# Optimization experiments

Measured on AMD Instinct MI355X. Metric: run time of the kernel, lower is better.

## Reference

```python
import jax, jax.numpy as jnp
import numpy as np

N_NODES = 100000
N_EDGES = 3200000
N_GRAPHS = 512


def setup_inputs() -> dict:
    key = jax.random.key(0)
    ks = jax.random.split(key, 8)
    x = jax.random.normal(ks[0], (N_NODES, 3), dtype=jnp.float32)
    W1 = jax.random.normal(ks[1], (3, 32), dtype=jnp.float32) * (1.0 / np.sqrt(3))
    b1 = jnp.zeros((32,), dtype=jnp.float32)
    W2 = jax.random.normal(ks[2], (32, 64), dtype=jnp.float32) * (1.0 / np.sqrt(32))
    b2 = jnp.zeros((64,), dtype=jnp.float32)
    W3 = jax.random.normal(ks[3], (64, 64), dtype=jnp.float32) * (1.0 / np.sqrt(64))
    b3 = jnp.zeros((64,), dtype=jnp.float32)
    Wc = jax.random.normal(ks[4], (128, 2), dtype=jnp.float32) * (1.0 / np.sqrt(128))
    bc = jnp.zeros((2,), dtype=jnp.float32)
    edge_index = jax.random.randint(ks[5], (2, N_EDGES), 0, N_NODES, dtype=jnp.int64)
    # sorted, evenly-split graph assignment -> every graph non-empty (needed for max pool)
    batch = (jnp.arange(N_NODES, dtype=jnp.int64) * N_GRAPHS) // N_NODES
    return {"x": x, "W1": W1, "b1": b1, "W2": W2, "b2": b2, "W3": W3, "b3": b3,
            "Wc": Wc, "bc": bc, "edge_index": edge_index, "batch": batch}


def _gcn_norm(edge_index, n_nodes):
    # add self loops, then symmetric normalization: deg^-1/2[src]*deg^-1/2[dst]
    loops = jnp.arange(n_nodes, dtype=edge_index.dtype)
    src = jnp.concatenate([edge_index[0], loops])
    dst = jnp.concatenate([edge_index[1], loops])
    deg = jax.ops.segment_sum(jnp.ones_like(dst, dtype=jnp.float32), dst,
                              num_segments=n_nodes)
    dinv = jax.lax.rsqrt(deg)  # deg >= 1 thanks to self loops
    norm = dinv[src] * dinv[dst]
    return src, dst, norm


def _gcn_conv(x, W, b, src, dst, norm, n_nodes):
    h = x @ W                                   # [N, out]
    msg = h[src] * norm[:, None]                # gather + edge scale  [E, out]
    agg = jax.ops.segment_sum(msg, dst, num_segments=n_nodes)  # scatter-add
    return agg + b


def reference(x, W1, b1, W2, b2, W3, b3, Wc, bc, edge_index, batch):
    n = x.shape[0]
    src, dst, norm = _gcn_norm(edge_index, n)
    h = jax.nn.relu(_gcn_conv(x, W1, b1, src, dst, norm, n))
    h = jax.nn.relu(_gcn_conv(h, W2, b2, src, dst, norm, n))
    h = _gcn_conv(h, W3, b3, src, dst, norm, n)
    # global max / mean pool over graphs
    x_max = jax.ops.segment_max(h, batch, num_segments=N_GRAPHS)
    sums = jax.ops.segment_sum(h, batch, num_segments=N_GRAPHS)
    cnts = jax.ops.segment_sum(jnp.ones((n, 1), dtype=h.dtype), batch,
                               num_segments=N_GRAPHS)
    x_mean = sums / jnp.maximum(cnts, 1.0)
    x_comb = jnp.concatenate([x_max, x_mean], axis=1)   # [G, 128]
    logits = x_comb @ Wc + bc                           # [G, 2]
    return jax.nn.softmax(logits, axis=1)
```

## Files before the change

### kernel.cpp

```cpp
#include <hip/hip_runtime.h>
#include <math.h>

#define TPB 256
#define TPB_H 512
#define TPB_BIN 1024
#define CSR_TPB 1024
#define NB_MAX 512
#define BKT_SHIFT 8
#define BKT_NODES 256
#define BIN_CHUNK 8192

__device__ inline float bfLO(unsigned u) { return __uint_as_float(u << 16); }
__device__ inline float bfHI(unsigned u) { return __uint_as_float(u & 0xffff0000u); }
__device__ inline unsigned short f2bf(float f) {
    unsigned int x = __float_as_uint(f);
    return (unsigned short)((x + 0x7fffu + ((x >> 16) & 1u)) >> 16);
}

__global__ void k_hist_coarse(const int* __restrict__ dst, int* __restrict__ bucketCnt,
                              int e, int nb) {
    __shared__ int h[NB_MAX];
    for (int i = threadIdx.x; i < nb; i += TPB_H) h[i] = 0;
    __syncthreads();
    int e4 = e >> 2;
    const int4* d4 = (const int4*)dst;
    for (long long i = (long long)blockIdx.x * TPB_H + threadIdx.x; i < e4;
         i += (long long)gridDim.x * TPB_H) {
        int4 v = d4[i];
        atomicAdd(&h[v.x >> BKT_SHIFT], 1);
        atomicAdd(&h[v.y >> BKT_SHIFT], 1);
        atomicAdd(&h[v.z >> BKT_SHIFT], 1);
        atomicAdd(&h[v.w >> BKT_SHIFT], 1);
    }
    if (blockIdx.x == 0)
        for (int i = (e4 << 2) + threadIdx.x; i < e; i += TPB_H)
            atomicAdd(&h[dst[i] >> BKT_SHIFT], 1);
    __syncthreads();
    for (int i = threadIdx.x; i < nb; i += TPB_H)
        if (h[i]) atomicAdd(&bucketCnt[i], h[i]);
}

__global__ void k_scanb(const int* __restrict__ cnt, int* __restrict__ boff,
                        int* __restrict__ bcur, int* __restrict__ off_nodes,
                        int nb, int e, int n) {
    __shared__ int lds[NB_MAX];
    int t = threadIdx.x;
    int v = (t < nb) ? cnt[t] : 0;
    lds[t] = v;
    __syncthreads();
    for (int d = 1; d < NB_MAX; d <<= 1) {
// ... 57 lines not shown
        if (t < BKT_NODES && t >= d) x = offl[t - d];
        __syncthreads();
        if (t < BKT_NODES) offl[t] += x;
        __syncthreads();
    }
    if (t < BKT_NODES) {
        int excl = offl[t] - v;
        cur[t] = excl;
        int nd = nbase + t;
        if (nd < n) {
            off_nodes[nd] = e0 + excl;
            dinv[nd] = rsqrtf((float)(v + 1));
        }
    }
    __syncthreads();
    for (int e = e0 + t; e < e1; e += CSR_TPB) {
        unsigned p = pairs[e];
        int l = (int)(p >> 24);
        int pos = e0 + atomicAdd(&cur[l], 1);
        csr[pos] = (int)(p & 0xffffffu);
    }
}

__global__ void k_scale3(const float* __restrict__ x, const float* __restrict__ dinv,
                         float* __restrict__ xp, int n3) {
    int t = blockIdx.x * TPB + threadIdx.x;
    if (t >= n3) return;
    xp[t] = x[t] * dinv[t / 3];
}

__global__ void k_g3mm1(const int* __restrict__ off, const int* __restrict__ csr,
                        const float* __restrict__ dinv, const float* __restrict__ xp,
                        const float* __restrict__ W1, const float* __restrict__ b1,
                        unsigned short* __restrict__ T1, int n) {
    __shared__ float w1s[96];
    __shared__ float b1s[32];
    if (threadIdx.x < 96) w1s[threadIdx.x] = W1[threadIdx.x];
    if (threadIdx.x < 32) b1s[threadIdx.x] = b1[threadIdx.x];
    __syncthreads();
    int i = blockIdx.x * TPB + threadIdx.x;
    if (i >= n) return;
    float s0 = xp[i * 3], s1 = xp[i * 3 + 1], s2 = xp[i * 3 + 2];
    int e = off[i], e1 = off[i + 1];
    for (; e + 3 < e1; e += 4) {
        int sa = csr[e], sb = csr[e + 1], sc = csr[e + 2], sd = csr[e + 3];
        float a0 = xp[sa * 3], a1 = xp[sa * 3 + 1], a2 = xp[sa * 3 + 2];
        float c0 = xp[sb * 3], c1 = xp[sb * 3 + 1], c2 = xp[sb * 3 + 2];
        float d0 = xp[sc * 3], d1 = xp[sc * 3 + 1], d2 = xp[sc * 3 + 2];
        float f0 = xp[sd * 3], f1 = xp[sd * 3 + 1], f2 = xp[sd * 3 + 2];
        s0 += a0 + c0 + d0 + f0;
        s1 += a1 + c1 + d1 + f1;
        s2 += a2 + c2 + d2 + f2;
    }
    for (; e < e1; ++e) {
        int s = csr[e];
        s0 += xp[s * 3]; s1 += xp[s * 3 + 1]; s2 += xp[s * 3 + 2];
    }
    float di = dinv[i];
    s0 *= di; s1 *= di; s2 *= di;
    unsigned outw[16];
#pragma unroll
    for (int fp = 0; fp < 16; fp++) {
        float h0 = fmaf(s0, w1s[2 * fp], fmaf(s1, w1s[32 + 2 * fp], fmaf(s2, w1s[64 + 2 * fp], b1s[2 * fp])));
        float h1 = fmaf(s0, w1s[2 * fp + 1], fmaf(s1, w1s[32 + 2 * fp + 1], fmaf(s2, w1s[64 + 2 * fp + 1], b1s[2 * fp + 1])));
        h0 = fmaxf(h0, 0.0f) * di;
        h1 = fmaxf(h1, 0.0f) * di;
        outw[fp] = (unsigned)f2bf(h0) | ((unsigned)f2bf(h1) << 16);
    }
    uint4* o = (uint4*)(T1 + (size_t)i * 32);
    o[0] = make_uint4(outw[0], outw[1], outw[2], outw[3]);
    o[1] = make_uint4(outw[4], outw[5], outw[6], outw[7]);
    o[2] = make_uint4(outw[8], outw[9], outw[10], outw[11]);
    o[3] = make_uint4(outw[12], outw[13], outw[14], outw[15]);
}

#define ACC8(v) do { \
    a0 += bfLO((v).x); a1 += bfHI((v).x); a2 += bfLO((v).y); a3 += bfHI((v).y); \
    a4 += bfLO((v).z); a5 += bfHI((v).z); a6 += bfLO((v).w); a7 += bfHI((v).w); } while (0)

__global__ void k_gather32b(const int* __restrict__ off, const int* __restrict__ csr,
                            const float* __restrict__ dinv, const unsigned short* __restrict__ T,
                            float* __restrict__ G, int n) {
    int w = (blockIdx.x * TPB + threadIdx.x) >> 6;
    if (w >= n) return;
    int lane = threadIdx.x & 63;
    int grp = lane >> 2, q = lane & 3;
    float a0 = 0, a1 = 0, a2 = 0, a3 = 0, a4 = 0, a5 = 0, a6 = 0, a7 = 0;
    if (grp == 0) {
        uint4 v = *(const uint4*)(T + ((size_t)w << 5) + (q << 3));
        ACC8(v);
    }
    int e = off[w] + grp, e1 = off[w + 1];
    for (; e + 16 < e1; e += 32) {
        int s0 = csr[e], s1 = csr[e + 16];
        uint4 v0 = *(const uint4*)(T + ((size_t)s0 << 5) + (q << 3));
        uint4 v1 = *(const uint4*)(T + ((size_t)s1 << 5) + (q << 3));
        ACC8(v0); ACC8(v1);
    }
    if (e < e1) {
        int s = csr[e];
        uint4 v = *(const uint4*)(T + ((size_t)s << 5) + (q << 3));
        ACC8(v);
    }
#pragma unroll
    for (int m = 4; m < 64; m <<= 1) {
        a0 += __shfl_xor(a0, m); a1 += __shfl_xor(a1, m);
        a2 += __shfl_xor(a2, m); a3 += __shfl_xor(a3, m);
        a4 += __shfl_xor(a4, m); a5 += __shfl_xor(a5, m);
        a6 += __shfl_xor(a6, m); a7 += __shfl_xor(a7, m);
    }
    if (grp == 0) {
        float di = dinv[w];
        float* g = G + ((size_t)w << 5) + (q << 3);
        *(float4*)g = make_float4(a0 * di, a1 * di, a2 * di, a3 * di);
        *(float4*)(g + 4) = make_float4(a4 * di, a5 * di, a6 * di, a7 * di);
    }
}

__global__ void k_mm2(const float* __restrict__ G, const float* __restrict__ W,
                      const float* __restrict__ b, const float* __restrict__ dinv,
                      unsigned short* __restrict__ T, int n) {
    int i = blockIdx.x * TPB + threadIdx.x;
    if (i >= n) return;
    float gr[32];
    const float4* g4 = (const float4*)(G + (size_t)i * 32);
#pragma unroll
    for (int c = 0; c < 8; c++) {
        float4 v = g4[c];
        gr[4 * c] = v.x; gr[4 * c + 1] = v.y; gr[4 * c + 2] = v.z; gr[4 * c + 3] = v.w;
    }
    float di = dinv[i];
    uint2* o = (uint2*)(T + (size_t)i * 64);
    for (int fc = 0; fc < 16; fc++) {
        const float* bb = b + 4 * fc;
        float a0 = bb[0], a1 = bb[1], a2 = bb[2], a3 = bb[3];
#pragma unroll
        for (int k = 0; k < 32; k++) {
            const float* wr = W + k * 64 + 4 * fc;
            float g = gr[k];
            a0 = fmaf(g, wr[0], a0);
            a1 = fmaf(g, wr[1], a1);
            a2 = fmaf(g, wr[2], a2);
            a3 = fmaf(g, wr[3], a3);
        }
        a0 = fmaxf(a0, 0.0f) * di; a1 = fmaxf(a1, 0.0f) * di;
        a2 = fmaxf(a2, 0.0f) * di; a3 = fmaxf(a3, 0.0f) * di;
        o[fc] = make_uint2((unsigned)f2bf(a0) | ((unsigned)f2bf(a1) << 16),
                           (unsigned)f2bf(a2) | ((unsigned)f2bf(a3) << 16));
    }
}

__global__ void k_gather64b(const int* __restrict__ off, const int* __restrict__ csr,
                            const float* __restrict__ dinv, const unsigned short* __restrict__ T,
                            float* __restrict__ G, int n) {
    int w = (blockIdx.x * TPB + threadIdx.x) >> 6;
    if (w >= n) return;
    int lane = threadIdx.x & 63;
    int grp = lane >> 3, q = lane & 7;
    float a0 = 0, a1 = 0, a2 = 0, a3 = 0, a4 = 0, a5 = 0, a6 = 0, a7 = 0;
    if (grp == 0) {
        uint4 v = *(const uint4*)(T + ((size_t)w << 6) + (q << 3));
        ACC8(v);
    }
    int e = off[w] + grp, e1 = off[w + 1];
    for (; e + 24 < e1; e += 32) {
        int s0 = csr[e], s1 = csr[e + 8], s2 = csr[e + 16], s3 = csr[e + 24];
        uint4 v0 = *(const uint4*)(T + ((size_t)s0 << 6) + (q << 3));
        uint4 v1 = *(const uint4*)(T + ((size_t)s1 << 6) + (q << 3));
        uint4 v2 = *(const uint4*)(T + ((size_t)s2 << 6) + (q << 3));
        uint4 v3 = *(const uint4*)(T + ((size_t)s3 << 6) + (q << 3));
        ACC8(v0); ACC8(v1); ACC8(v2); ACC8(v3);
    }
    for (; e < e1; e += 8) {
        int s = csr[e];
        uint4 v = *(const uint4*)(T + ((size_t)s << 6) + (q << 3));
        ACC8(v);
    }
#pragma unroll
    for (int m = 8; m < 64; m <<= 1) {
        a0 += __shfl_xor(a0, m); a1 += __shfl_xor(a1, m);
        a2 += __shfl_xor(a2, m); a3 += __shfl_xor(a3, m);
        a4 += __shfl_xor(a4, m); a5 += __shfl_xor(a5, m);
        a6 += __shfl_xor(a6, m); a7 += __shfl_xor(a7, m);
    }
    if (grp == 0) {
        float di = dinv[w];
        float* g = G + ((size_t)w << 6) + (q << 3);
        *(float4*)g = make_float4(a0 * di, a1 * di, a2 * di, a3 * di);
        *(float4*)(g + 4) = make_float4(a4 * di, a5 * di, a6 * di, a7 * di);
    }
}

__global__ void k_mm3(const float* __restrict__ G, const float* __restrict__ W,
                      const float* __restrict__ b, float* __restrict__ H, int n) {
    int i = blockIdx.x * TPB + threadIdx.x;
    if (i >= n) return;
    float gr[64];
    const float4* g4 = (const float4*)(G + (size_t)i * 64);
#pragma unroll
    for (int c = 0; c < 16; c++) {
        float4 v = g4[c];
        gr[4 * c] = v.x; gr[4 * c + 1] = v.y; gr[4 * c + 2] = v.z; gr[4 * c + 3] = v.w;
    }
    float4* h4 = (float4*)(H + (size_t)i * 64);
    for (int fc = 0; fc < 16; fc++) {
        const float* bb = b + 4 * fc;
        float a0 = bb[0], a1 = bb[1], a2 = bb[2], a3 = bb[3];
#pragma unroll
        for (int k = 0; k < 64; k++) {
            const float* wr = W + k * 64 + 4 * fc;
            float g = gr[k];
            a0 = fmaf(g, wr[0], a0);
            a1 = fmaf(g, wr[1], a1);
            a2 = fmaf(g, wr[2], a2);
            a3 = fmaf(g, wr[3], a3);
        }
        h4[fc] = make_float4(a0, a1, a2, a3);
    }
}

__global__ void k_pool(const float* __restrict__ H, const float* __restrict__ Wc,
                       const float* __restrict__ bc, float* __restrict__ out,
                       int n, int g_total) {
    int g = blockIdx.x;
    int f = threadIdx.x & 63;
    int c = threadIdx.x >> 6;
    long long start = ((long long)g * n + g_total - 1) / g_total;
    long long end = ((long long)(g + 1) * n + g_total - 1) / g_total;
    float mx = -INFINITY, sm = 0.0f;
    for (long long i = start + c; i < end; i += 4) {
        float v = H[(i << 6) | f];
        mx = fmaxf(mx, v);
        sm += v;
    }
    __shared__ float smax[4][64], ssum[4][64], slog[2];
    smax[c][f] = mx; ssum[c][f] = sm;
    __syncthreads();
    if (c == 0) {
        mx = fmaxf(fmaxf(smax[0][f], smax[1][f]), fmaxf(smax[2][f], smax[3][f]));
        sm = ssum[0][f] + ssum[1][f] + ssum[2][f] + ssum[3][f];
        long long cnt = end - start;
        smax[0][f] = mx;
        ssum[0][f] = sm / (float)(cnt > 0 ? cnt : 1);
    }
    __syncthreads();
    if (threadIdx.x < 2) {
        int cls = threadIdx.x;
        float l = bc[cls];
        for (int k = 0; k < 64; k++)
            l += smax[0][k] * Wc[k * 2 + cls] + ssum[0][k] * Wc[(64 + k) * 2 + cls];
        slog[cls] = l;
    }
    __syncthreads();
    if (threadIdx.x == 0) {
        float m = fmaxf(slog[0], slog[1]);
        float e0 = expf(slog[0] - m), e1 = expf(slog[1] - m);
        float inv = 1.0f / (e0 + e1);
        out[g * 2 + 0] = e0 * inv;
        out[g * 2 + 1] = e1 * inv;
    }
}

extern "C" void kernel_launch(void* const* d_in, const int* in_sizes, int n_in,
                              void* d_out, int out_size, void* d_ws, size_t ws_size,
                              hipStream_t stream) {
    const float* x  = (const float*)d_in[0];
    const float* W1 = (const float*)d_in[1];
    const float* b1 = (const float*)d_in[2];
    const float* W2 = (const float*)d_in[3];
    const float* b2 = (const float*)d_in[4];
    const float* W3 = (const float*)d_in[5];
    const float* b3 = (const float*)d_in[6];
    const float* Wc = (const float*)d_in[7];
    const float* bc = (const float*)d_in[8];
    const int*   ei = (const int*)d_in[9];

    const int N = in_sizes[0] / 3;
    const int E = in_sizes[9] / 2;
    const int G = out_size / 2;
    const int* src = ei;
    const int* dst = ei + E;

    char* ws = (char*)d_ws;
    size_t off_b = 0;
    auto alloc = [&](size_t bytes) {
        size_t o = off_b;
        off_b = (off_b + bytes + 255) & ~(size_t)255;
        return (void*)(ws + o);
    };
    float* dinv      = (float*)alloc((size_t)N * 4);
    int*   off       = (int*)alloc((size_t)(N + 1) * 4);
    int*   bucketCnt = (int*)alloc((NB_MAX + 1) * 4);
    int*   bucketOff = (int*)alloc((NB_MAX + 1) * 4);
    int*   bucketCur = (int*)alloc((NB_MAX + 1) * 4);
    int*   csr       = (int*)alloc((size_t)E * 4);
    float* xp        = (float*)alloc((size_t)N * 3 * 4);
    size_t bufA_sz   = (size_t)N * 64 * 4;
    if ((size_t)E * 4 > bufA_sz) bufA_sz = (size_t)E * 4;
    float* bufA      = (float*)alloc(bufA_sz);
    float* bufB      = (float*)alloc((size_t)N * 64 * 4);

    unsigned* pairs = (unsigned*)bufA;
    float* G1 = bufA;
    float* G2 = bufA;
    unsigned short* T1 = (unsigned short*)bufB;
    unsigned short* T2 = (unsigned short*)bufB;
    float* H  = bufB;

    auto cdiv = [](long long a, long long b) { return (int)((a + b - 1) / b); };
    const int nb = cdiv(N, BKT_NODES);

    hipMemsetAsync(bucketCnt, 0, (size_t)nb * 4, stream);
    k_hist_coarse<<<1024, TPB_H, 0, stream>>>(dst, bucketCnt, E, nb);
    k_scanb<<<1, NB_MAX, 0, stream>>>(bucketCnt, bucketOff, bucketCur, off, nb, E, N);
    k_bin_pairs<<<cdiv(E, BIN_CHUNK), TPB_BIN, 0, stream>>>(src, dst, bucketCur, pairs, E, nb);
    k_bucket_csr<<<nb, CSR_TPB, 0, stream>>>(pairs, bucketOff, off, dinv, csr, N);

    k_scale3<<<cdiv((long long)N * 3, TPB), TPB, 0, stream>>>(x, dinv, xp, N * 3);
    k_g3mm1<<<cdiv(N, TPB), TPB, 0, stream>>>(off, csr, dinv, xp, W1, b1, T1, N);

    k_gather32b<<<cdiv((long long)N * 64, TPB), TPB, 0, stream>>>(off, csr, dinv, T1, G1, N);
    k_mm2<<<cdiv(N, TPB), TPB, 0, stream>>>(G1, W2, b2, dinv, T2, N);

    k_gather64b<<<cdiv((long long)N * 64, TPB), TPB, 0, stream>>>(off, csr, dinv, T2, G2, N);
    k_mm3<<<cdiv(N, TPB), TPB, 0, stream>>>(G2, W3, b3, H, N);

    k_pool<<<G, TPB, 0, stream>>>(H, Wc, bc, (float*)d_out, N, G);
}
```

Measured before the change: 307.6 us.

## Quantize gathered GCN features to per-row int8 with float scales

Intermediate node features fed to the two neighbour-gather kernels are now stored as unsigned 8-bit values with a per-node float scale instead of bf16, halving the bytes fetched per edge. The gather kernels are reorganised so each lane reads 16 bytes covering 16 features, with fewer lanes per row and more edges in flight per wavefront. Each gathered row now also needs an extra scale load and integer-to-float conversions. Accuracy drops to 7-bit per-row quantization, which may or may not stay within tolerance.

```diff
diff --git a/kernel.cpp b/kernel.cpp
--- a/kernel.cpp
+++ b/kernel.cpp
@@ -9,13 +9,6 @@
 #define BKT_SHIFT 8
 #define BKT_NODES 256
 #define BIN_CHUNK 8192
-
-__device__ inline float bfLO(unsigned u) { return __uint_as_float(u << 16); }
-__device__ inline float bfHI(unsigned u) { return __uint_as_float(u & 0xffff0000u); }
-__device__ inline unsigned short f2bf(float f) {
-    unsigned int x = __float_as_uint(f);
-    return (unsigned short)((x + 0x7fffu + ((x >> 16) & 1u)) >> 16);
-}
 
 __global__ void k_hist_coarse(const int* __restrict__ dst, int* __restrict__ bucketCnt,
                               int e, int nb) {
@@ -139,7 +132,7 @@
 __global__ void k_g3mm1(const int* __restrict__ off, const int* __restrict__ csr,
                         const float* __restrict__ dinv, const float* __restrict__ xp,
                         const float* __restrict__ W1, const float* __restrict__ b1,
-                        unsigned short* __restrict__ T1, int n) {
+                        unsigned char* __restrict__ T1, float* __restrict__ sc1, int n) {
     __shared__ float w1s[96];
     __shared__ float b1s[32];
     if (threadIdx.x < 96) w1s[threadIdx.x] = W1[threadIdx.x];
@@ -165,68 +158,80 @@
     }
     float di = dinv[i];
     s0 *= di; s1 *= di; s2 *= di;
-    unsigned outw[16];
-#pragma unroll
-    for (int fp = 0; fp < 16; fp++) {
-        float h0 = fmaf(s0, w1s[2 * fp], fmaf(s1, w1s[32 + 2 * fp], fmaf(s2, w1s[64 + 2 * fp], b1s[2 * fp])));
-        float h1 = fmaf(s0, w1s[2 * fp + 1], fmaf(s1, w1s[32 + 2 * fp + 1], fmaf(s2, w1s[64 + 2 * fp + 1], b1s[2 * fp + 1])));
-        h0 = fmaxf(h0, 0.0f) * di;
-        h1 = fmaxf(h1, 0.0f) * di;
-        outw[fp] = (unsigned)f2bf(h0) | ((unsigned)f2bf(h1) << 16);
+    float vals[32];
+    float mx = 0.0f;
+#pragma unroll
+    for (int f = 0; f < 32; f++) {
+        float h = fmaf(s0, w1s[f], fmaf(s1, w1s[32 + f], fmaf(s2, w1s[64 + f], b1s[f])));
+        h = fmaxf(h, 0.0f) * di;
+        vals[f] = h;
+        mx = fmaxf(mx, h);
+    }
+    float inv = 127.0f / fmaxf(mx, 1e-20f);
+    sc1[i] = mx * (1.0f / 127.0f);
+    unsigned pw[8];
+#pragma unroll
+    for (int u = 0; u < 8; u++) {
+        unsigned q0 = (unsigned)__float2int_rn(vals[4 * u] * inv);
+        unsigned q1 = (unsigned)__float2int_rn(vals[4 * u + 1] * inv);
+        unsigned q2 = (unsigned)__float2int_rn(vals[4 * u + 2] * inv);
+        unsigned q3 = (unsigned)__float2int_rn(vals[4 * u + 3] * inv);
+        pw[u] = q0 | (q1 << 8) | (q2 << 16) | (q3 << 24);
     }
     uint4* o = (uint4*)(T1 + (size_t)i * 32);
-    o[0] = make_uint4(outw[0], outw[1], outw[2], outw[3]);
-    o[1] = make_uint4(outw[4], outw[5], outw[6], outw[7]);
-    o[2] = make_uint4(outw[8], outw[9], outw[10], outw[11]);
-    o[3] = make_uint4(outw[12], outw[13], outw[14], outw[15]);
-}
-
-#define ACC8(v) do { \
-    a0 += bfLO((v).x); a1 += bfHI((v).x); a2 += bfLO((v).y); a3 += bfHI((v).y); \
-    a4 += bfLO((v).z); a5 += bfHI((v).z); a6 += bfLO((v).w); a7 += bfHI((v).w); } while (0)
-
-__global__ void k_gather32b(const int* __restrict__ off, const int* __restrict__ csr,
-                            const float* __restrict__ dinv, const unsigned short* __restrict__ T,
-                            float* __restrict__ G, int n) {
+    o[0] = make_uint4(pw[0], pw[1], pw[2], pw[3]);
+    o[1] = make_uint4(pw[4], pw[5], pw[6], pw[7]);
+}
+
+#define QACC4(word, base) do { \
+    a[(base) + 0] = fmaf(s, (float)((word) & 0xffu), a[(base) + 0]); \
+    a[(base) + 1] = fmaf(s, (float)(((word) >> 8) & 0xffu), a[(base) + 1]); \
+    a[(base) + 2] = fmaf(s, (float)(((word) >> 16) & 0xffu), a[(base) + 2]); \
+    a[(base) + 3] = fmaf(s, (float)((word) >> 24), a[(base) + 3]); \
+} while (0)
+
+#define QACC16(v) do { QACC4((v).x, 0); QACC4((v).y, 4); QACC4((v).z, 8); QACC4((v).w, 12); } while (0)
+
+__global__ void k_gather32i(const int* __restrict__ off, const int* __restrict__ csr,
+                            const float* __restrict__ dinv, const unsigned char* __restrict__ T,
+                            const float* __restrict__ sc, float* __restrict__ G, int n) {
     int w = (blockIdx.x * TPB + threadIdx.x) >> 6;
     if (w >= n) return;
     int lane = threadIdx.x & 63;
-    int grp = lane >> 2, q = lane & 3;
-    float a0 = 0, a1 = 0, a2 = 0, a3 = 0, a4 = 0, a5 = 0, a6 = 0, a7 = 0;
+    int grp = lane >> 1, q = lane & 1;
+    float a[16];
+#pragma unroll
+    for (int j = 0; j < 16; j++) a[j] = 0.0f;
     if (grp == 0) {
-        uint4 v = *(const uint4*)(T + ((size_t)w << 5) + (q << 3));
-        ACC8(v);
+        float s = sc[w];
+        uint4 v = *(const uint4*)(T + ((size_t)w << 5) + (q << 4));
+        QACC16(v);
     }
     int e = off[w] + grp, e1 = off[w + 1];
-    for (; e + 16 < e1; e += 32) {
-        int s0 = csr[e], s1 = csr[e + 16];
-        uint4 v0 = *(const uint4*)(T + ((size_t)s0 << 5) + (q << 3));
-        uint4 v1 = *(const uint4*)(T + ((size_t)s1 << 5) + (q << 3));
-        ACC8(v0); ACC8(v1);
-    }
-    if (e < e1) {
-        int s = csr[e];
-        uint4 v = *(const uint4*)(T + ((size_t)s << 5) + (q << 3));
-        ACC8(v);
-    }
-#pragma unroll
-    for (int m = 4; m < 64; m <<= 1) {
-        a0 += __shfl_xor(a0, m); a1 += __shfl_xor(a1, m);
-        a2 += __shfl_xor(a2, m); a3 += __shfl_xor(a3, m);
-        a4 += __shfl_xor(a4, m); a5 += __shfl_xor(a5, m);
-        a6 += __shfl_xor(a6, m); a7 += __shfl_xor(a7, m);
+    for (; e < e1; e += 32) {
+        int si = csr[e];
+        float s = sc[si];
+        uint4 v = *(const uint4*)(T + ((size_t)si << 5) + (q << 4));
+        QACC16(v);
+    }
+#pragma unroll
+    for (int m = 2; m < 64; m <<= 1) {
+#pragma unroll
+        for (int j = 0; j < 16; j++) a[j] += __shfl_xor(a[j], m);
     }
     if (grp == 0) {
         float di = dinv[w];
-        float* g = G + ((size_t)w << 5) + (q << 3);
-        *(float4*)g = make_float4(a0 * di, a1 * di, a2 * di, a3 * di);
-        *(float4*)(g + 4) = make_float4(a4 * di, a5 * di, a6 * di, a7 * di);
+        float4* g = (float4*)(G + ((size_t)w << 5) + (q << 4));
+#pragma unroll
+        for (int c = 0; c < 4; c++)
+            g[c] = make_float4(a[4 * c] * di, a[4 * c + 1] * di,
+                               a[4 * c + 2] * di, a[4 * c + 3] * di);
     }
 }
 
 __global__ void k_mm2(const float* __restrict__ G, const float* __restrict__ W,
                       const float* __restrict__ b, const float* __restrict__ dinv,
-                      unsigned short* __restrict__ T, int n) {
+                      unsigned char* __restrict__ T, float* __restrict__ sc2, int n) {
     int i = blockIdx.x * TPB + threadIdx.x;
     if (i >= n) return;
     float gr[32];
@@ -237,7 +242,9 @@
         gr[4 * c] = v.x; gr[4 * c + 1] = v.y; gr[4 * c + 2] = v.z; gr[4 * c + 3] = v.w;
     }
     float di = dinv[i];
-    uint2* o = (uint2*)(T + (size_t)i * 64);
+    float vals[64];
+    float mx = 0.0f;
+#pragma unroll
     for (int fc = 0; fc < 16; fc++) {
         const float* bb = b + 4 * fc;
         float a0 = bb[0], a1 = bb[1], a2 = bb[2], a3 = bb[3];
@@ -252,49 +259,70 @@
         }
         a0 = fmaxf(a0, 0.0f) * di; a1 = fmaxf(a1, 0.0f) * di;
         a2 = fmaxf(a2, 0.0f) * di; a3 = fmaxf(a3, 0.0f) * di;
-        o[fc] = make_uint2((unsigned)f2bf(a0) | ((unsigned)f2bf(a1) << 16),
-                           (unsigned)f2bf(a2) | ((unsigned)f2bf(a3) << 16));
-    }
-}
-
-__global__ void k_gather64b(const int* __restrict__ off, const int* __restrict__ csr,
-                            const float* __restrict__ dinv, const unsigned short* __restrict__ T,
-                            float* __restrict__ G, int n) {
+        vals[4 * fc] = a0; vals[4 * fc + 1] = a1;
+        vals[4 * fc + 2] = a2; vals[4 * fc + 3] = a3;
+        mx = fmaxf(mx, fmaxf(fmaxf(a0, a1), fmaxf(a2, a3)));
+    }
+    float inv = 127.0f / fmaxf(mx, 1e-20f);
+    sc2[i] = mx * (1.0f / 127.0f);
+    unsigned pw[16];
+#pragma unroll
+    for (int u = 0; u < 16; u++) {
+        unsigned q0 = (unsigned)__float2int_rn(vals[4 * u] * inv);
+        unsigned q1 = (unsigned)__float2int_rn(vals[4 * u + 1] * inv);
+        unsigned q2 = (unsigned)__float2int_rn(vals[4 * u + 2] * inv);
+        unsigned q3 = (unsigned)__float2int_rn(vals[4 * u + 3] * inv);
+        pw[u] = q0 | (q1 << 8) | (q2 << 16) | (q3 << 24);
+    }
+    uint4* o = (uint4*)(T + (size_t)i * 64);
+    o[0] = make_uint4(pw[0], pw[1], pw[2], pw[3]);
+    o[1] = make_uint4(pw[4], pw[5], pw[6], pw[7]);
+    o[2] = make_uint4(pw[8], pw[9], pw[10], pw[11]);
+    o[3] = make_uint4(pw[12], pw[13], pw[14], pw[15]);
+}
+
+__global__ void k_gather64i(const int* __restrict__ off, const int* __restrict__ csr,
+                            const float* __restrict__ dinv, const unsigned char* __restrict__ T,
+                            const float* __restrict__ sc, float* __restrict__ G, int n) {
     int w = (blockIdx.x * TPB + threadIdx.x) >> 6;
     if (w >= n) return;
     int lane = threadIdx.x & 63;
-    int grp = lane >> 3, q = lane & 7;
-    float a0 = 0, a1 = 0, a2 = 0, a3 = 0, a4 = 0, a5 = 0, a6 = 0, a7 = 0;
+    int grp = lane >> 2, q = lane & 3;
+    float a[16];
+#pragma unroll
+    for (int j = 0; j < 16; j++) a[j] = 0.0f;
     if (grp == 0) {
-        uint4 v = *(const uint4*)(T + ((size_t)w << 6) + (q << 3));
-        ACC8(v);
+        float s = sc[w];
+        uint4 v = *(const uint4*)(T + ((size_t)w << 6) + (q << 4));
+        QACC16(v);
     }
     int e = off[w] + grp, e1 = off[w + 1];
-    for (; e + 24 < e1; e += 32) {
-        int s0 = csr[e], s1 = csr[e + 8], s2 = csr[e + 16], s3 = csr[e + 24];
-        uint4 v0 = *(const uint4*)(T + ((size_t)s0 << 6) + (q << 3));
-        uint4 v1 = *(const uint4*)(T + ((size_t)s1 << 6) + (q << 3));
-        uint4 v2 = *(const uint4*)(T + ((size_t)s2 << 6) + (q << 3));
-        uint4 v3 = *(const uint4*)(T + ((size_t)s3 << 6) + (q << 3));
-        ACC8(v0); ACC8(v1); ACC8(v2); ACC8(v3);
-    }
-    for (; e < e1; e += 8) {
-        int s = csr[e];
-        uint4 v = *(const uint4*)(T + ((size_t)s << 6) + (q << 3));
-        ACC8(v);
-    }
-#pragma unroll
-    for (int m = 8; m < 64; m <<= 1) {
-        a0 += __shfl_xor(a0, m); a1 += __shfl_xor(a1, m);
-        a2 += __shfl_xor(a2, m); a3 += __shfl_xor(a3, m);
-        a4 += __shfl_xor(a4, m); a5 += __shfl_xor(a5, m);
-        a6 += __shfl_xor(a6, m); a7 += __shfl_xor(a7, m);
+    for (; e + 16 < e1; e += 32) {
+        int s0i = csr[e], s1i = csr[e + 16];
+        float sA = sc[s0i], sB = sc[s1i];
+        uint4 v0 = *(const uint4*)(T + ((size_t)s0i << 6) + (q << 4));
+        uint4 v1 = *(const uint4*)(T + ((size_t)s1i << 6) + (q << 4));
+        { float s = sA; QACC16(v0); }
+        { float s = sB; QACC16(v1); }
+    }
+    if (e < e1) {
+        int si = csr[e];
+        float s = sc[si];
+        uint4 v = *(const uint4*)(T + ((size_t)si << 6) + (q << 4));
+        QACC16(v);
+    }
+#pragma unroll
+    for (int m = 4; m < 64; m <<= 1) {
+#pragma unroll
+        for (int j = 0; j < 16; j++) a[j] += __shfl_xor(a[j], m);
     }
     if (grp == 0) {
         float di = dinv[w];
-        float* g = G + ((size_t)w << 6) + (q << 3);
-        *(float4*)g = make_float4(a0 * di, a1 * di, a2 * di, a3 * di);
-        *(float4*)(g + 4) = make_float4(a4 * di, a5 * di, a6 * di, a7 * di);
+        float4* g = (float4*)(G + ((size_t)w << 6) + (q << 4));
+#pragma unroll
+        for (int c = 0; c < 4; c++)
+            g[c] = make_float4(a[4 * c] * di, a[4 * c + 1] * di,
+                               a[4 * c + 2] * di, a[4 * c + 3] * di);
     }
 }
 
@@ -402,6 +430,8 @@
     int*   bucketCur = (int*)alloc((NB_MAX + 1) * 4);
     int*   csr       = (int*)alloc((size_t)E * 4);
     float* xp        = (float*)alloc((size_t)N * 3 * 4);
+    float* sc1       = (float*)alloc((size_t)N * 4);
+    float* sc2       = (float*)alloc((size_t)N * 4);
     size_t bufA_sz   = (size_t)N * 64 * 4;
     if ((size_t)E * 4 > bufA_sz) bufA_sz = (size_t)E * 4;
     float* bufA      = (float*)alloc(bufA_sz);
@@ -410,9 +440,9 @@
     unsigned* pairs = (unsigned*)bufA;
     float* G1 = bufA;
     float* G2 = bufA;
-    unsigned short* T1 = (unsigned short*)bufB;
-    unsigned short* T2 = (unsigned short*)bufB;
-    float* H  = bufB;
+    unsigned char* T1 = (unsigned char*)bufB;
+    unsigned char* T2 = (unsigned char*)bufB;
+    float* H  = (float*)bufB;
 
     auto cdiv = [](long long a, long long b) { return (int)((a + b - 1) / b); };
     const int nb = cdiv(N, BKT_NODES);
@@ -424,12 +454,12 @@
     k_bucket_csr<<<nb, CSR_TPB, 0, stream>>>(pairs, bucketOff, off, dinv, csr, N);
 
     k_scale3<<<cdiv((long long)N * 3, TPB), TPB, 0, stream>>>(x, dinv, xp, N * 3);
-    k_g3mm1<<<cdiv(N, TPB), TPB, 0, stream>>>(off, csr, dinv, xp, W1, b1, T1, N);
-
-    k_gather32b<<<cdiv((long long)N * 64, TPB), TPB, 0, stream>>>(off, csr, dinv, T1, G1, N);
-    k_mm2<<<cdiv(N, TPB), TPB, 0, stream>>>(G1, W2, b2, dinv, T2, N);
-
-    k_gather64b<<<cdiv((long long)N * 64, TPB), TPB, 0, stream>>>(off, csr, dinv, T2, G2, N);
+    k_g3mm1<<<cdiv(N, TPB), TPB, 0, stream>>>(off, csr, dinv, xp, W1, b1, T1, sc1, N);
+
+    k_gather32i<<<cdiv((long long)N * 64, TPB), TPB, 0, stream>>>(off, csr, dinv, T1, sc1, G1, N);
+    k_mm2<<<cdiv(N, TPB), TPB, 0, stream>>>(G1, W2, b2, dinv, T2, sc2, N);
+
+    k_gather64i<<<cdiv((long long)N * 64, TPB), TPB, 0, stream>>>(off, csr, dinv, T2, sc2, G2, N);
     k_mm3<<<cdiv(N, TPB), TPB, 0, stream>>>(G2, W3, b3, H, N);
 
     k_pool<<<G, TPB, 0, stream>>>(H, Wc, bc, (float*)d_out, N, G);
```

After: 339.7 us. +10.4%, slower.

## Quantize layer-2 features to int8 with per-node scale and fuse pooling into mm3

Applied to the files above, without the earlier changes.

Layer-2 node features are now stored as int8 with a per-node scale instead of bf16, which halves the bytes each edge gather reads in the 64-wide aggregation. The third matmul is fused with global max/mean pooling through shared-memory and global atomics, so the N×64 hidden buffer is never written to memory or read back. A small classifier kernel then finishes the softmax. Int8 quantization adds error and float atomic sums make the result order-dependent.

```diff
diff --git a/kernel.cpp b/kernel.cpp
--- a/kernel.cpp
+++ b/kernel.cpp
@@ -15,6 +15,14 @@
 __device__ inline unsigned short f2bf(float f) {
     unsigned int x = __float_as_uint(f);
     return (unsigned short)((x + 0x7fffu + ((x >> 16) & 1u)) >> 16);
+}
+__device__ inline unsigned fkey(float f) {
+    int s = __float_as_int(f);
+    return (unsigned)(s >= 0 ? (s | 0x80000000) : ~s);
+}
+__device__ inline float funkey(unsigned k) {
+    int s = (k & 0x80000000u) ? (int)(k & 0x7fffffffu) : ~(int)k;
+    return __int_as_float(s);
 }
 
 __global__ void k_hist_coarse(const int* __restrict__ dst, int* __restrict__ bucketCnt,
@@ -226,7 +234,7 @@
 
 __global__ void k_mm2(const float* __restrict__ G, const float* __restrict__ W,
                       const float* __restrict__ b, const float* __restrict__ dinv,
-                      unsigned short* __restrict__ T, int n) {
+                      unsigned char* __restrict__ T, float* __restrict__ sc2, int n) {
     int i = blockIdx.x * TPB + threadIdx.x;
     if (i >= n) return;
     float gr[32];
@@ -237,7 +245,9 @@
         gr[4 * c] = v.x; gr[4 * c + 1] = v.y; gr[4 * c + 2] = v.z; gr[4 * c + 3] = v.w;
     }
     float di = dinv[i];
-    uint2* o = (uint2*)(T + (size_t)i * 64);
+    float vals[64];
+    float mx = 0.0f;
+#pragma unroll
     for (int fc = 0; fc < 16; fc++) {
         const float* bb = b + 4 * fc;
         float a0 = bb[0], a1 = bb[1], a2 = bb[2], a3 = bb[3];
@@ -252,114 +262,156 @@
         }
         a0 = fmaxf(a0, 0.0f) * di; a1 = fmaxf(a1, 0.0f) * di;
         a2 = fmaxf(a2, 0.0f) * di; a3 = fmaxf(a3, 0.0f) * di;
-        o[fc] = make_uint2((unsigned)f2bf(a0) | ((unsigned)f2bf(a1) << 16),
-                           (unsigned)f2bf(a2) | ((unsigned)f2bf(a3) << 16));
-    }
-}
-
-__global__ void k_gather64b(const int* __restrict__ off, const int* __restrict__ csr,
-                            const float* __restrict__ dinv, const unsigned short* __restrict__ T,
-                            float* __restrict__ G, int n) {
+        vals[4 * fc] = a0; vals[4 * fc + 1] = a1;
+        vals[4 * fc + 2] = a2; vals[4 * fc + 3] = a3;
+        mx = fmaxf(mx, fmaxf(fmaxf(a0, a1), fmaxf(a2, a3)));
+    }
+    float inv = 127.0f / fmaxf(mx, 1e-20f);
+    sc2[i] = mx * (1.0f / 127.0f);
+    unsigned pw[16];
+#pragma unroll
+    for (int u = 0; u < 16; u++) {
+        unsigned q0 = (unsigned)__float2int_rn(vals[4 * u] * inv);
+        unsigned q1 = (unsigned)__float2int_rn(vals[4 * u + 1] * inv);
+        unsigned q2 = (unsigned)__float2int_rn(vals[4 * u + 2] * inv);
+        unsigned q3 = (unsigned)__float2int_rn(vals[4 * u + 3] * inv);
+        pw[u] = q0 | (q1 << 8) | (q2 << 16) | (q3 << 24);
+    }
+    uint4* o = (uint4*)(T + (size_t)i * 64);
+    o[0] = make_uint4(pw[0], pw[1], pw[2], pw[3]);
+    o[1] = make_uint4(pw[4], pw[5], pw[6], pw[7]);
+    o[2] = make_uint4(pw[8], pw[9], pw[10], pw[11]);
+    o[3] = make_uint4(pw[12], pw[13], pw[14], pw[15]);
+}
+
+#define QACC4(word, base) do { \
+    a[(base) + 0] = fmaf(s, (float)((word) & 0xffu), a[(base) + 0]); \
+    a[(base) + 1] = fmaf(s, (float)(((word) >> 8) & 0xffu), a[(base) + 1]); \
+    a[(base) + 2] = fmaf(s, (float)(((word) >> 16) & 0xffu), a[(base) + 2]); \
+    a[(base) + 3] = fmaf(s, (float)((word) >> 24), a[(base) + 3]); \
+} while (0)
+
+#define QACC16(v) do { QACC4((v).x, 0); QACC4((v).y, 4); QACC4((v).z, 8); QACC4((v).w, 12); } while (0)
+
+__global__ void k_gather64i(const int* __restrict__ off, const int* __restrict__ csr,
+                            const float* __restrict__ dinv, const unsigned char* __restrict__ T,
+                            const float* __restrict__ sc, float* __restrict__ G, int n) {
     int w = (blockIdx.x * TPB + threadIdx.x) >> 6;
     if (w >= n) return;
     int lane = threadIdx.x & 63;
-    int grp = lane >> 3, q = lane & 7;
-    float a0 = 0, a1 = 0, a2 = 0, a3 = 0, a4 = 0, a5 = 0, a6 = 0, a7 = 0;
+    int grp = lane >> 2, q = lane & 3;
+    float a[16];
+#pragma unroll
+    for (int j = 0; j < 16; j++) a[j] = 0.0f;
     if (grp == 0) {
-        uint4 v = *(const uint4*)(T + ((size_t)w << 6) + (q << 3));
-        ACC8(v);
+        float s = sc[w];
+        uint4 v = *(const uint4*)(T + ((size_t)w << 6) + (q << 4));
+        QACC16(v);
     }
     int e = off[w] + grp, e1 = off[w + 1];
-    for (; e + 24 < e1; e += 32) {
-        int s0 = csr[e], s1 = csr[e + 8], s2 = csr[e + 16], s3 = csr[e + 24];
-        uint4 v0 = *(const uint4*)(T + ((size_t)s0 << 6) + (q << 3));
-        uint4 v1 = *(const uint4*)(T + ((size_t)s1 << 6) + (q << 3));
-        uint4 v2 = *(const uint4*)(T + ((size_t)s2 << 6) + (q << 3));
-        uint4 v3 = *(const uint4*)(T + ((size_t)s3 << 6) + (q << 3));
-        ACC8(v0); ACC8(v1); ACC8(v2); ACC8(v3);
-    }
-    for (; e < e1; e += 8) {
-        int s = csr[e];
-        uint4 v = *(const uint4*)(T + ((size_t)s << 6) + (q << 3));
-        ACC8(v);
-    }
-#pragma unroll
-    for (int m = 8; m < 64; m <<= 1) {
-        a0 += __shfl_xor(a0, m); a1 += __shfl_xor(a1, m);
-        a2 += __shfl_xor(a2, m); a3 += __shfl_xor(a3, m);
-        a4 += __shfl_xor(a4, m); a5 += __shfl_xor(a5, m);
-        a6 += __shfl_xor(a6, m); a7 += __shfl_xor(a7, m);
+    for (; e + 16 < e1; e += 32) {
+        int s0i = csr[e], s1i = csr[e + 16];
+        float sA = sc[s0i], sB = sc[s1i];
+        uint4 v0 = *(const uint4*)(T + ((size_t)s0i << 6) + (q << 4));
+        uint4 v1 = *(const uint4*)(T + ((size_t)s1i << 6) + (q << 4));
+        { float s = sA; QACC16(v0); }
+        { float s = sB; QACC16(v1); }
+    }
+    if (e < e1) {
+        int si = csr[e];
+        float s = sc[si];
+        uint4 v = *(const uint4*)(T + ((size_t)si << 6) + (q << 4));
+        QACC16(v);
+    }
+#pragma unroll
+    for (int m = 4; m < 64; m <<= 1) {
+#pragma unroll
+        for (int j = 0; j < 16; j++) a[j] += __shfl_xor(a[j], m);
     }
     if (grp == 0) {
         float di = dinv[w];
-        float* g = G + ((size_t)w << 6) + (q << 3);
-        *(float4*)g = make_float4(a0 * di, a1 * di, a2 * di, a3 * di);
-        *(float4*)(g + 4) = make_float4(a4 * di, a5 * di, a6 * di, a7 * di);
-    }
-}
-
-__global__ void k_mm3(const float* __restrict__ G, const float* __restrict__ W,
-                      const float* __restrict__ b, float* __restrict__ H, int n) {
-    int i = blockIdx.x * TPB + threadIdx.x;
-    if (i >= n) return;
-    float gr[64];
-    const float4* g4 = (const float4*)(G + (size_t)i * 64);
-#pragma unroll
-    for (int c = 0; c < 16; c++) {
-        float4 v = g4[c];
-        gr[4 * c] = v.x; gr[4 * c + 1] = v.y; gr[4 * c + 2] = v.z; gr[4 * c + 3] = v.w;
-    }
-    float4* h4 = (float4*)(H + (size_t)i * 64);
-    for (int fc = 0; fc < 16; fc++) {
-        const float* bb = b + 4 * fc;
-        float a0 = bb[0], a1 = bb[1], a2 = bb[2], a3 = bb[3];
-#pragma unroll
-        for (int k = 0; k < 64; k++) {
-            const float* wr = W + k * 64 + 4 * fc;
-            float g = gr[k];
-            a0 = fmaf(g, wr[0], a0);
-            a1 = fmaf(g, wr[1], a1);
-            a2 = fmaf(g, wr[2], a2);
-            a3 = fmaf(g, wr[3], a3);
+        float4* g = (float4*)(G + ((size_t)w << 6) + (q << 4));
+#pragma unroll
+        for (int c = 0; c < 4; c++)
+            g[c] = make_float4(a[4 * c] * di, a[4 * c + 1] * di,
+                               a[4 * c + 2] * di, a[4 * c + 3] * di);
+    }
+}
+
+__global__ void k_mm3pool(const float* __restrict__ G, const float* __restrict__ W,
+                          const float* __restrict__ b, unsigned* __restrict__ gmaxk,
+                          float* __restrict__ gsum, int n, int g_total) {
+    __shared__ unsigned lmk[4][64];
+    __shared__ float lsm[4][64];
+    int t = threadIdx.x;
+    int i0 = blockIdx.x * TPB;
+    int i = i0 + t;
+    int gfirst = (int)(((long long)i0 * g_total) / n);
+    lmk[t >> 6][t & 63] = 0u;
+    lsm[t >> 6][t & 63] = 0.0f;
+    __syncthreads();
+    if (i < n) {
+        float gr[64];
+        const float4* g4 = (const float4*)(G + (size_t)i * 64);
+#pragma unroll
+        for (int c = 0; c < 16; c++) {
+            float4 v = g4[c];
+            gr[4 * c] = v.x; gr[4 * c + 1] = v.y; gr[4 * c + 2] = v.z; gr[4 * c + 3] = v.w;
         }
-        h4[fc] = make_float4(a0, a1, a2, a3);
-    }
-}
-
-__global__ void k_pool(const float* __restrict__ H, const float* __restrict__ Wc,
-                       const float* __restrict__ bc, float* __restrict__ out,
-                       int n, int g_total) {
+        int gl = (int)(((long long)i * g_total) / n) - gfirst;
+        for (int fc = 0; fc < 16; fc++) {
+            const float* bb = b + 4 * fc;
+            float a0 = bb[0], a1 = bb[1], a2 = bb[2], a3 = bb[3];
+#pragma unroll
+            for (int k = 0; k < 64; k++) {
+                const float* wr = W + k * 64 + 4 * fc;
+                float g = gr[k];
+                a0 = fmaf(g, wr[0], a0);
+                a1 = fmaf(g, wr[1], a1);
+                a2 = fmaf(g, wr[2], a2);
+                a3 = fmaf(g, wr[3], a3);
+            }
+            atomicMax(&lmk[gl][4 * fc + 0], fkey(a0));
+            atomicMax(&lmk[gl][4 * fc + 1], fkey(a1));
+            atomicMax(&lmk[gl][4 * fc + 2], fkey(a2));
+            atomicMax(&lmk[gl][4 * fc + 3], fkey(a3));
+            atomicAdd(&lsm[gl][4 * fc + 0], a0);
+            atomicAdd(&lsm[gl][4 * fc + 1], a1);
+            atomicAdd(&lsm[gl][4 * fc + 2], a2);
+            atomicAdd(&lsm[gl][4 * fc + 3], a3);
+        }
+    }
+    __syncthreads();
+    int sgl = t >> 6, sf = t & 63;
+    unsigned mk = lmk[sgl][sf];
+    float sm = lsm[sgl][sf];
+    if (mk != 0u) {
+        int g = gfirst + sgl;
+        atomicMax(&gmaxk[g * 64 + sf], mk);
+        atomicAdd(&gsum[g * 64 + sf], sm);
+    }
+}
+
+__global__ void k_cls(const unsigned* __restrict__ gmaxk, const float* __restrict__ gsum,
+                      const float* __restrict__ Wc, const float* __restrict__ bc,
+                      float* __restrict__ out, int n, int g_total) {
     int g = blockIdx.x;
-    int f = threadIdx.x & 63;
-    int c = threadIdx.x >> 6;
+    int f = threadIdx.x;
     long long start = ((long long)g * n + g_total - 1) / g_total;
     long long end = ((long long)(g + 1) * n + g_total - 1) / g_total;
-    float mx = -INFINITY, sm = 0.0f;
-    for (long long i = start + c; i < end; i += 4) {
-        float v = H[(i << 6) | f];
-        mx = fmaxf(mx, v);
-        sm += v;
-    }
-    __shared__ float smax[4][64], ssum[4][64], slog[2];
-    smax[c][f] = mx; ssum[c][f] = sm;
-    __syncthreads();
-    if (c == 0) {
-        mx = fmaxf(fmaxf(smax[0][f], smax[1][f]), fmaxf(smax[2][f], smax[3][f]));
-        sm = ssum[0][f] + ssum[1][f] + ssum[2][f] + ssum[3][f];
-        long long cnt = end - start;
-        smax[0][f] = mx;
-        ssum[0][f] = sm / (float)(cnt > 0 ? cnt : 1);
-    }
-    __syncthreads();
-    if (threadIdx.x < 2) {
-        int cls = threadIdx.x;
-        float l = bc[cls];
+    float cnt = (float)(end - start);
+    __shared__ float smax[64], smean[64], slog[2];
+    smax[f] = funkey(gmaxk[g * 64 + f]);
+    smean[f] = gsum[g * 64 + f] / fmaxf(cnt, 1.0f);
+    __syncthreads();
+    if (f < 2) {
+        float l = bc[f];
         for (int k = 0; k < 64; k++)
-            l += smax[0][k] * Wc[k * 2 + cls] + ssum[0][k] * Wc[(64 + k) * 2 + cls];
-        slog[cls] = l;
-    }
-    __syncthreads();
-    if (threadIdx.x == 0) {
+            l += smax[k] * Wc[k * 2 + f] + smean[k] * Wc[(64 + k) * 2 + f];
+        slog[f] = l;
+    }
+    __syncthreads();
+    if (f == 0) {
         float m = fmaxf(slog[0], slog[1]);
         float e0 = expf(slog[0] - m), e1 = expf(slog[1] - m);
         float inv = 1.0f / (e0 + e1);
@@ -395,24 +447,26 @@
         off_b = (off_b + bytes + 255) & ~(size_t)255;
         return (void*)(ws + o);
     };
-    float* dinv      = (float*)alloc((size_t)N * 4);
-    int*   off       = (int*)alloc((size_t)(N + 1) * 4);
-    int*   bucketCnt = (int*)alloc((NB_MAX + 1) * 4);
-    int*   bucketOff = (int*)alloc((NB_MAX + 1) * 4);
-    int*   bucketCur = (int*)alloc((NB_MAX + 1) * 4);
-    int*   csr       = (int*)alloc((size_t)E * 4);
-    float* xp        = (float*)alloc((size_t)N * 3 * 4);
-    size_t bufA_sz   = (size_t)N * 64 * 4;
+    float*    dinv      = (float*)alloc((size_t)N * 4);
+    int*      off       = (int*)alloc((size_t)(N + 1) * 4);
+    int*      bucketCnt = (int*)alloc((NB_MAX + 1) * 4);
+    int*      bucketOff = (int*)alloc((NB_MAX + 1) * 4);
+    int*      bucketCur = (int*)alloc((NB_MAX + 1) * 4);
+    int*      csr       = (int*)alloc((size_t)E * 4);
+    float*    xp        = (float*)alloc((size_t)N * 3 * 4);
+    float*    sc2       = (float*)alloc((size_t)N * 4);
+    unsigned* gmaxk     = (unsigned*)alloc((size_t)G * 64 * 4);
+    float*    gsum      = (float*)alloc((size_t)G * 64 * 4);
+    size_t bufA_sz = (size_t)N * 64 * 4;
     if ((size_t)E * 4 > bufA_sz) bufA_sz = (size_t)E * 4;
-    float* bufA      = (float*)alloc(bufA_sz);
-    float* bufB      = (float*)alloc((size_t)N * 64 * 4);
+    float* bufA = (float*)alloc(bufA_sz);
+    float* bufB = (float*)alloc((size_t)N * 64);
 
     unsigned* pairs = (unsigned*)bufA;
     float* G1 = bufA;
     float* G2 = bufA;
     unsigned short* T1 = (unsigned short*)bufB;
-    unsigned short* T2 = (unsigned short*)bufB;
-    float* H  = bufB;
+    unsigned char*  T2 = (unsigned char*)bufB;
 
     auto cdiv = [](long long a, long long b) { return (int)((a + b - 1) / b); };
     const int nb = cdiv(N, BKT_NODES);
@@ -427,10 +481,12 @@
     k_g3mm1<<<cdiv(N, TPB), TPB, 0, stream>>>(off, csr, dinv, xp, W1, b1, T1, N);
 
     k_gather32b<<<cdiv((long long)N * 64, TPB), TPB, 0, stream>>>(off, csr, dinv, T1, G1, N);
-    k_mm2<<<cdiv(N, TPB), TPB, 0, stream>>>(G1, W2, b2, dinv, T2, N);
-
-    k_gather64b<<<cdiv((long long)N * 64, TPB), TPB, 0, stream>>>(off, csr, dinv, T2, G2, N);
-    k_mm3<<<cdiv(N, TPB), TPB, 0, stream>>>(G2, W3, b3, H, N);
-
-    k_pool<<<G, TPB, 0, stream>>>(H, Wc, bc, (float*)d_out, N, G);
-}
+    k_mm2<<<cdiv(N, TPB), TPB, 0, stream>>>(G1, W2, b2, dinv, T2, sc2, N);
+
+    k_gather64i<<<cdiv((long long)N * 64, TPB), TPB, 0, stream>>>(off, csr, dinv, T2, sc2, G2, N);
+    hipMemsetAsync(gmaxk, 0, (size_t)G * 64 * 4, stream);
+    hipMemsetAsync(gsum, 0, (size_t)G * 64 * 4, stream);
+    k_mm3pool<<<cdiv(N, TPB), TPB, 0, stream>>>(G2, W3, b3, gmaxk, gsum, N, G);
+
+    k_cls<<<G, 64, 0, stream>>>(gmaxk, gsum, Wc, bc, (float*)d_out, N, G);
+}
```

Result: slower. 352.8 us (+14.7%).

## Quantize layer-3 gather features to uint8 with a global max scale

Applied to the files above, without the earlier changes.

Layer-2 outputs (post-ReLU, non-negative) are now quantized to 8-bit unsigned values. The scale comes from a global max that k_mm2 computes with a block reduction and atomicMax. A new k_quant kernel converts the bf16 features to uint8, and the 64-wide gather reads 8 bytes per lane instead of 16, then rescales once per node. This halves the bytes moved by the random-access gather over 3.2M edges. In exchange it adds an extra pass, an atomic, and a coarse precision loss that may hurt accuracy tolerance.

```diff
diff --git a/kernel.cpp b/kernel.cpp
--- a/kernel.cpp
+++ b/kernel.cpp
@@ -226,62 +226,98 @@
 
 __global__ void k_mm2(const float* __restrict__ G, const float* __restrict__ W,
                       const float* __restrict__ b, const float* __restrict__ dinv,
-                      unsigned short* __restrict__ T, int n) {
+                      unsigned short* __restrict__ T, unsigned* __restrict__ gmaxu, int n) {
     int i = blockIdx.x * TPB + threadIdx.x;
-    if (i >= n) return;
-    float gr[32];
-    const float4* g4 = (const float4*)(G + (size_t)i * 32);
-#pragma unroll
-    for (int c = 0; c < 8; c++) {
-        float4 v = g4[c];
-        gr[4 * c] = v.x; gr[4 * c + 1] = v.y; gr[4 * c + 2] = v.z; gr[4 * c + 3] = v.w;
-    }
-    float di = dinv[i];
-    uint2* o = (uint2*)(T + (size_t)i * 64);
-    for (int fc = 0; fc < 16; fc++) {
-        const float* bb = b + 4 * fc;
-        float a0 = bb[0], a1 = bb[1], a2 = bb[2], a3 = bb[3];
-#pragma unroll
-        for (int k = 0; k < 32; k++) {
-            const float* wr = W + k * 64 + 4 * fc;
-            float g = gr[k];
-            a0 = fmaf(g, wr[0], a0);
-            a1 = fmaf(g, wr[1], a1);
-            a2 = fmaf(g, wr[2], a2);
-            a3 = fmaf(g, wr[3], a3);
+    float mx = 0.0f;
+    if (i < n) {
+        float gr[32];
+        const float4* g4 = (const float4*)(G + (size_t)i * 32);
+#pragma unroll
+        for (int c = 0; c < 8; c++) {
+            float4 v = g4[c];
+            gr[4 * c] = v.x; gr[4 * c + 1] = v.y; gr[4 * c + 2] = v.z; gr[4 * c + 3] = v.w;
         }
-        a0 = fmaxf(a0, 0.0f) * di; a1 = fmaxf(a1, 0.0f) * di;
-        a2 = fmaxf(a2, 0.0f) * di; a3 = fmaxf(a3, 0.0f) * di;
-        o[fc] = make_uint2((unsigned)f2bf(a0) | ((unsigned)f2bf(a1) << 16),
-                           (unsigned)f2bf(a2) | ((unsigned)f2bf(a3) << 16));
-    }
-}
-
-__global__ void k_gather64b(const int* __restrict__ off, const int* __restrict__ csr,
-                            const float* __restrict__ dinv, const unsigned short* __restrict__ T,
-                            float* __restrict__ G, int n) {
+        float di = dinv[i];
+        uint2* o = (uint2*)(T + (size_t)i * 64);
+        for (int fc = 0; fc < 16; fc++) {
+            const float* bb = b + 4 * fc;
+            float a0 = bb[0], a1 = bb[1], a2 = bb[2], a3 = bb[3];
+#pragma unroll
+            for (int k = 0; k < 32; k++) {
+                const float* wr = W + k * 64 + 4 * fc;
+                float g = gr[k];
+                a0 = fmaf(g, wr[0], a0);
+                a1 = fmaf(g, wr[1], a1);
+                a2 = fmaf(g, wr[2], a2);
+                a3 = fmaf(g, wr[3], a3);
+            }
+            a0 = fmaxf(a0, 0.0f) * di; a1 = fmaxf(a1, 0.0f) * di;
+            a2 = fmaxf(a2, 0.0f) * di; a3 = fmaxf(a3, 0.0f) * di;
+            mx = fmaxf(mx, fmaxf(fmaxf(a0, a1), fmaxf(a2, a3)));
+            o[fc] = make_uint2((unsigned)f2bf(a0) | ((unsigned)f2bf(a1) << 16),
+                               (unsigned)f2bf(a2) | ((unsigned)f2bf(a3) << 16));
+        }
+    }
+#pragma unroll
+    for (int m = 1; m < 64; m <<= 1) mx = fmaxf(mx, __shfl_xor(mx, m));
+    __shared__ float wmax[4];
+    if ((threadIdx.x & 63) == 0) wmax[threadIdx.x >> 6] = mx;
+    __syncthreads();
+    if (threadIdx.x == 0) {
+        float m4 = fmaxf(fmaxf(wmax[0], wmax[1]), fmaxf(wmax[2], wmax[3]));
+        atomicMax(gmaxu, __float_as_uint(m4));
+    }
+}
+
+__global__ void k_quant(const unsigned short* __restrict__ Tp, const unsigned* __restrict__ gmaxu,
+                        unsigned char* __restrict__ Tq, int n8) {
+    int j = blockIdx.x * TPB + threadIdx.x;
+    if (j >= n8) return;
+    float gm = __uint_as_float(gmaxu[0]);
+    float inv = 254.0f / fmaxf(gm, 1e-20f);
+    uint4 v = *(const uint4*)(Tp + (size_t)j * 8);
+    unsigned q0 = (unsigned)__float2int_rn(bfLO(v.x) * inv);
+    unsigned q1 = (unsigned)__float2int_rn(bfHI(v.x) * inv);
+    unsigned q2 = (unsigned)__float2int_rn(bfLO(v.y) * inv);
+    unsigned q3 = (unsigned)__float2int_rn(bfHI(v.y) * inv);
+    unsigned q4 = (unsigned)__float2int_rn(bfLO(v.z) * inv);
+    unsigned q5 = (unsigned)__float2int_rn(bfHI(v.z) * inv);
+    unsigned q6 = (unsigned)__float2int_rn(bfLO(v.w) * inv);
+    unsigned q7 = (unsigned)__float2int_rn(bfHI(v.w) * inv);
+    *(uint2*)(Tq + (size_t)j * 8) =
+        make_uint2(q0 | (q1 << 8) | (q2 << 16) | (q3 << 24),
+                   q4 | (q5 << 8) | (q6 << 16) | (q7 << 24));
+}
+
+#define UACC8(v) do { \
+    a0 += (float)((v).x & 0xffu); a1 += (float)(((v).x >> 8) & 0xffu); \
+    a2 += (float)(((v).x >> 16) & 0xffu); a3 += (float)((v).x >> 24); \
+    a4 += (float)((v).y & 0xffu); a5 += (float)(((v).y >> 8) & 0xffu); \
+    a6 += (float)(((v).y >> 16) & 0xffu); a7 += (float)((v).y >> 24); } while (0)
+
+__global__ void k_gather64q(const int* __restrict__ off, const int* __restrict__ csr,
+                            const float* __restrict__ dinv, const unsigned char* __restrict__ T,
+                            const unsigned* __restrict__ gmaxu, float* __restrict__ G, int n) {
     int w = (blockIdx.x * TPB + threadIdx.x) >> 6;
     if (w >= n) return;
     int lane = threadIdx.x & 63;
     int grp = lane >> 3, q = lane & 7;
     float a0 = 0, a1 = 0, a2 = 0, a3 = 0, a4 = 0, a5 = 0, a6 = 0, a7 = 0;
     if (grp == 0) {
-        uint4 v = *(const uint4*)(T + ((size_t)w << 6) + (q << 3));
-        ACC8(v);
+        uint2 v = *(const uint2*)(T + ((size_t)w << 6) + (q << 3));
+        UACC8(v);
     }
     int e = off[w] + grp, e1 = off[w + 1];
-    for (; e + 24 < e1; e += 32) {
-        int s0 = csr[e], s1 = csr[e + 8], s2 = csr[e + 16], s3 = csr[e + 24];
-        uint4 v0 = *(const uint4*)(T + ((size_t)s0 << 6) + (q << 3));
-        uint4 v1 = *(const uint4*)(T + ((size_t)s1 << 6) + (q << 3));
-        uint4 v2 = *(const uint4*)(T + ((size_t)s2 << 6) + (q << 3));
-        uint4 v3 = *(const uint4*)(T + ((size_t)s3 << 6) + (q << 3));
-        ACC8(v0); ACC8(v1); ACC8(v2); ACC8(v3);
-    }
-    for (; e < e1; e += 8) {
+    for (; e + 8 < e1; e += 16) {
+        int s0 = csr[e], s1 = csr[e + 8];
+        uint2 v0 = *(const uint2*)(T + ((size_t)s0 << 6) + (q << 3));
+        uint2 v1 = *(const uint2*)(T + ((size_t)s1 << 6) + (q << 3));
+        UACC8(v0); UACC8(v1);
+    }
+    if (e < e1) {
         int s = csr[e];
-        uint4 v = *(const uint4*)(T + ((size_t)s << 6) + (q << 3));
-        ACC8(v);
+        uint2 v = *(const uint2*)(T + ((size_t)s << 6) + (q << 3));
+        UACC8(v);
     }
 #pragma unroll
     for (int m = 8; m < 64; m <<= 1) {
@@ -291,10 +327,11 @@
         a6 += __shfl_xor(a6, m); a7 += __shfl_xor(a7, m);
     }
     if (grp == 0) {
-        float di = dinv[w];
+        float gm = __uint_as_float(gmaxu[0]);
+        float s = dinv[w] * (gm * (1.0f / 254.0f));
         float* g = G + ((size_t)w << 6) + (q << 3);
-        *(float4*)g = make_float4(a0 * di, a1 * di, a2 * di, a3 * di);
-        *(float4*)(g + 4) = make_float4(a4 * di, a5 * di, a6 * di, a7 * di);
+        *(float4*)g = make_float4(a0 * s, a1 * s, a2 * s, a3 * s);
+        *(float4*)(g + 4) = make_float4(a4 * s, a5 * s, a6 * s, a7 * s);
     }
 }
 
@@ -395,29 +432,32 @@
         off_b = (off_b + bytes + 255) & ~(size_t)255;
         return (void*)(ws + o);
     };
-    float* dinv      = (float*)alloc((size_t)N * 4);
-    int*   off       = (int*)alloc((size_t)(N + 1) * 4);
-    int*   bucketCnt = (int*)alloc((NB_MAX + 1) * 4);
-    int*   bucketOff = (int*)alloc((NB_MAX + 1) * 4);
-    int*   bucketCur = (int*)alloc((NB_MAX + 1) * 4);
-    int*   csr       = (int*)alloc((size_t)E * 4);
-    float* xp        = (float*)alloc((size_t)N * 3 * 4);
-    size_t bufA_sz   = (size_t)N * 64 * 4;
+    float*    dinv      = (float*)alloc((size_t)N * 4);
+    int*      off       = (int*)alloc((size_t)(N + 1) * 4);
+    int*      bucketCnt = (int*)alloc((NB_MAX + 1) * 4);
+    int*      bucketOff = (int*)alloc((NB_MAX + 1) * 4);
+    int*      bucketCur = (int*)alloc((NB_MAX + 1) * 4);
+    int*      csr       = (int*)alloc((size_t)E * 4);
+    float*    xp        = (float*)alloc((size_t)N * 3 * 4);
+    unsigned* gmaxu     = (unsigned*)alloc(256);
+    size_t bufA_sz = (size_t)N * 64 * 4;
     if ((size_t)E * 4 > bufA_sz) bufA_sz = (size_t)E * 4;
-    float* bufA      = (float*)alloc(bufA_sz);
-    float* bufB      = (float*)alloc((size_t)N * 64 * 4);
+    float* bufA = (float*)alloc(bufA_sz);
+    float* bufB = (float*)alloc((size_t)N * 64 * 4);
 
     unsigned* pairs = (unsigned*)bufA;
     float* G1 = bufA;
     float* G2 = bufA;
-    unsigned short* T1 = (unsigned short*)bufB;
-    unsigned short* T2 = (unsigned short*)bufB;
-    float* H  = bufB;
+    unsigned short* T1  = (unsigned short*)bufB;
+    unsigned short* T2p = (unsigned short*)bufB;
+    unsigned char*  T2q = (unsigned char*)bufB + (size_t)N * 128;
+    float* H = (float*)bufB;
 
     auto cdiv = [](long long a, long long b) { return (int)((a + b - 1) / b); };
     const int nb = cdiv(N, BKT_NODES);
 
     hipMemsetAsync(bucketCnt, 0, (size_t)nb * 4, stream);
+    hipMemsetAsync(gmaxu, 0, 4, stream);
     k_hist_coarse<<<1024, TPB_H, 0, stream>>>(dst, bucketCnt, E, nb);
     k_scanb<<<1, NB_MAX, 0, stream>>>(bucketCnt, bucketOff, bucketCur, off, nb, E, N);
     k_bin_pairs<<<cdiv(E, BIN_CHUNK), TPB_BIN, 0, stream>>>(src, dst, bucketCur, pairs, E, nb);
@@ -427,9 +467,10 @@
     k_g3mm1<<<cdiv(N, TPB), TPB, 0, stream>>>(off, csr, dinv, xp, W1, b1, T1, N);
 
     k_gather32b<<<cdiv((long long)N * 64, TPB), TPB, 0, stream>>>(off, csr, dinv, T1, G1, N);
-    k_mm2<<<cdiv(N, TPB), TPB, 0, stream>>>(G1, W2, b2, dinv, T2, N);
-
-    k_gather64b<<<cdiv((long long)N * 64, TPB), TPB, 0, stream>>>(off, csr, dinv, T2, G2, N);
+    k_mm2<<<cdiv(N, TPB), TPB, 0, stream>>>(G1, W2, b2, dinv, T2p, gmaxu, N);
+
+    k_quant<<<cdiv((long long)N * 8, TPB), TPB, 0, stream>>>(T2p, gmaxu, T2q, N * 8);
+    k_gather64q<<<cdiv((long long)N * 64, TPB), TPB, 0, stream>>>(off, csr, dinv, T2q, gmaxu, G2, N);
     k_mm3<<<cdiv(N, TPB), TPB, 0, stream>>>(G2, W3, b3, H, N);
 
     k_pool<<<G, TPB, 0, stream>>>(H, Wc, bc, (float*)d_out, N, G);
```

New measurement: 296.5 us. 3.6% less time.
